# Performance work log

Hardware: AMD Instinct MI355X
Metric: run time of the kernel (lower is better)

## Reference

```python
import jax, jax.numpy as jnp
import numpy as np

N, F_IN, C, H, L = 4096, 768, 256, 4, 2
DH = C // H  # 64 per-head dim for GATv2


def _ln(x, g, b, eps=1e-5):
    mu = x.mean(-1, keepdims=True)
    var = ((x - mu) ** 2).mean(-1, keepdims=True)
    return (x - mu) / jnp.sqrt(var + eps) * g + b


def _gat_layer(x, wl, wr, att, b, src, dst):
    # GATv2Conv: e_ij = att . leaky_relu(Wl x_j + Wr x_i); softmax over incoming j; concat heads.
    xs = (x @ wl).reshape(N, H, DH)  # source transform
    xd = (x @ wr).reshape(N, H, DH)  # target transform
    e = jnp.einsum('ehd,hd->eh', jax.nn.leaky_relu(xs[src] + xd[dst], 0.2), att)  # [E,H]
    m = jax.ops.segment_max(e, dst, num_segments=N)          # segment softmax (stable)
    p = jnp.exp(e - m[dst])
    s = jax.ops.segment_sum(p, dst, num_segments=N)
    alpha = p / (s[dst] + 1e-16)                             # [E,H]
    out = jax.ops.segment_sum(alpha[:, :, None] * xs[src], dst, num_segments=N)
    return out.reshape(N, C) + b


def _mha(x, wq, wk, wv, bq, bk, bv, wo, bo):
    # nn.MultiheadAttention, batch=1 sequence of all news nodes, eval mode.
    q = (x @ wq + bq).reshape(N, H, DH)
    k = (x @ wk + bk).reshape(N, H, DH)
    v = (x @ wv + bv).reshape(N, H, DH)
    scale = np.float32(1.0 / np.sqrt(DH))
    a = jax.nn.softmax(jnp.einsum('nhd,mhd->hnm', q, k) * scale, axis=-1)  # [H,N,N]
    o = jnp.einsum('hnm,mhd->nhd', a, v).reshape(N, C)
    return o @ wo + bo


def setup_inputs() -> dict:
    key = jax.random.key(0)
    ks = jax.random.split(key, 32)
    rn = lambda k, shp: (jax.random.normal(k, shp, dtype=jnp.float32) * 0.02)
    inp = {
        'x': jax.random.normal(ks[0], (N, F_IN), dtype=jnp.float32),
        'edge_index': jax.random.randint(ks[1], (2, N * 64), 0, N, dtype=jnp.int64),
        'emb_w': rn(ks[2], (F_IN, C)), 'emb_b': jnp.zeros((C,), jnp.float32),
        'g1_wl': rn(ks[3], (C, C)), 'g1_wr': rn(ks[4], (C, C)),
        'g1_att': rn(ks[5], (H, DH)), 'g1_b': jnp.zeros((C,), jnp.float32),
        'g2_wl': rn(ks[6], (C, C)), 'g2_wr': rn(ks[7], (C, C)),
        'g2_att': rn(ks[8], (H, DH)), 'g2_b': jnp.zeros((C,), jnp.float32),
        'mha_wq': rn(ks[9], (C, C)), 'mha_wk': rn(ks[10], (C, C)), 'mha_wv': rn(ks[11], (C, C)),
        'mha_bq': jnp.zeros((C,), jnp.float32), 'mha_bk': jnp.zeros((C,), jnp.float32),
        'mha_bv': jnp.zeros((C,), jnp.float32),
        'mha_wo': rn(ks[12], (C, C)), 'mha_bo': jnp.zeros((C,), jnp.float32),
        'ln_g': jnp.ones((C,), jnp.float32), 'ln_b': jnp.zeros((C,), jnp.float32),
        'cls_w1': rn(ks[13], (C, C // 2)), 'cls_b1': jnp.zeros((C // 2,), jnp.float32),
        'cls_w2': rn(ks[14], (C // 2, 2)), 'cls_b2': jnp.zeros((2,), jnp.float32),
    }
    return inp


def reference(x, edge_index, emb_w, emb_b, g1_wl, g1_wr, g1_att, g1_b,
              g2_wl, g2_wr, g2_att, g2_b, mha_wq, mha_wk, mha_wv, mha_bq,
              mha_bk, mha_bv, mha_wo, mha_bo, ln_g, ln_b,
              cls_w1, cls_b1, cls_w2, cls_b2):
    # add self loops (GATv2Conv default add_self_loops=True)
    loops = jnp.arange(N, dtype=edge_index.dtype)
    src = jnp.concatenate([edge_index[0], loops])
    dst = jnp.concatenate([edge_index[1], loops])

    h = x @ emb_w + emb_b                              # node embedding Linear(-1, C)
    h = jax.nn.relu(_gat_layer(h, g1_wl, g1_wr, g1_att, g1_b, src, dst))
    h = jax.nn.relu(_gat_layer(h, g2_wl, g2_wr, g2_att, g2_b, src, dst))

    # entity-aware self-attention + residual LayerNorm
    enh = _mha(h, mha_wq, mha_wk, mha_wv, mha_bq, mha_bk, mha_bv, mha_wo, mha_bo)
    h = _ln(h + enh, ln_g, ln_b)

    # classifier MLP (dropout = identity in eval)
    h = jax.nn.relu(h @ cls_w1 + cls_b1)
    return h @ cls_w2 + cls_b2
```

## Files before the change

kernel.cpp:

```cpp
#include <hip/hip_runtime.h>

typedef __attribute__((ext_vector_type(8))) short short8_t;
typedef __attribute__((ext_vector_type(4))) short short4_t;
typedef __attribute__((ext_vector_type(4))) float f32x4_t;

#define N_NODES  4096
#define E0_EDGES 262144
#define E_TOTAL  266240
#define SPLITS   8
#define KV_PER_SPLIT (N_NODES / SPLITS)

__device__ __forceinline__ float bf2f(unsigned short u){
  union { unsigned int i; float f; } v; v.i = ((unsigned int)u) << 16; return v.f;
}
__device__ __forceinline__ unsigned short f2bf(float f){
  union { float f; unsigned int i; } v; v.f = f;
  unsigned int r = (v.i + 0x7FFFu + ((v.i >> 16) & 1u)) >> 16;
  return (unsigned short)r;
}
__device__ __forceinline__ unsigned int cvtpk_bf16(float lo, float hi){
  unsigned int r;
  asm volatile("v_cvt_pk_bf16_f32 %0, %1, %2" : "=v"(r) : "v"(lo), "v"(hi));
  return r;
}
template<int CTRL>
__device__ __forceinline__ float dpp_add(float x){
  int v = __builtin_amdgcn_update_dpp(0, __float_as_int(x), CTRL, 0xF, 0xF, true);
  return x + __int_as_float(v);
}
__device__ __forceinline__ float rowsum16(float x){
  x = dpp_add<0xB1>(x); x = dpp_add<0x4E>(x); x = dpp_add<0x124>(x); x = dpp_add<0x128>(x);
  return x;
}
__device__ __forceinline__ void wg_barrier(){
  asm volatile("s_waitcnt lgkmcnt(0)" ::: "memory");
  __builtin_amdgcn_s_barrier();
  asm volatile("" ::: "memory");
}
__device__ __forceinline__ f32x4_t mfma16(short4_t a, short4_t b, f32x4_t c){
  asm("v_mfma_f32_16x16x16_bf16 %0, %1, %2, %0" : "+v"(c) : "v"(a), "v"(b));
  return c;
}

struct TJob { const float* src; unsigned short* dst; int rows, cols, tile0; };
struct TJobs { TJob j[10]; };

__global__ __launch_bounds__(256) void prep_kernel(const float* __restrict__ x, unsigned short* __restrict__ xb,
                                                   TJobs jobs, int tb, int* __restrict__ zp){
  __shared__ unsigned short tile[64 * 64];
  int b = blockIdx.x, t = threadIdx.x;
  if (b < 3072){
    int i = (b * 256 + t) * 4;
    float4 v = *(const float4*)&x[i];
    union { unsigned short u[4]; uint2 q; } o;
    o.u[0] = f2bf(v.x); o.u[1] = f2bf(v.y); o.u[2] = f2bf(v.z); o.u[3] = f2bf(v.w);
    *(uint2*)&xb[i] = o.q;
    return;
  }
  if (b < 3072 + tb){
    int bb = b - 3072;
    int ji = 0;
    #pragma unroll
    for (int k = 1; k < 10; k++) if (bb >= jobs.j[k].tile0) ji = k;
    TJob J = jobs.j[ji];
    int lt = bb - J.tile0;
    int tpr = J.cols >> 6;
    int tr = lt / tpr, tc = lt - tr * tpr;
    #pragma unroll
    for (int i2 = 0; i2 < 2; i2++){
      int e = i2 * 2048 + t * 8;
      int nl = e >> 6, c8 = e & 63;
      const float* sp = &J.src[(size_t)(tr * 64 + nl) * J.cols + tc * 64 + c8];
      float4 v0 = *(const float4*)sp;
      float4 v1 = *(const float4*)(sp + 4);
      union { unsigned short u[8]; uint4 q; } o;
      o.u[0]=f2bf(v0.x); o.u[1]=f2bf(v0.y); o.u[2]=f2bf(v0.z); o.u[3]=f2bf(v0.w);
      o.u[4]=f2bf(v1.x); o.u[5]=f2bf(v1.y); o.u[6]=f2bf(v1.z); o.u[7]=f2bf(v1.w);
      *(uint4*)&tile[nl * 64 + (((c8 >> 3) ^ ((nl >> 3) & 7)) * 8)] = o.q;
    }
    __syncthreads();
    #pragma unroll
    for (int i2 = 0; i2 < 2; i2++){
      int e = i2 * 2048 + t * 8;
      int cl = e >> 6, n8 = e & 63;
      union { unsigned short u[8]; uint4 q; } o;
      #pragma unroll
      for (int j = 0; j < 8; j++){
        int row = n8 + j;
        o.u[j] = tile[row * 64 + (((cl >> 3) ^ ((row >> 3) & 7)) * 8) + (cl & 7)];
      }
      *(uint4*)&J.dst[(size_t)(tc * 64 + cl) * J.rows + tr * 64 + n8] = o.q;
    }
    return;
  }
  int i = (b - 3072 - tb) * 256 + t;
  if (i < 8192) zp[i] = 0;
}

__global__ __launch_bounds__(256) void scatter_kernel(const int* __restrict__ ei, const int* __restrict__ offs,
                                                      int* __restrict__ cur, int* __restrict__ csrc){
  int e = blockIdx.x * 256 + threadIdx.x;
  if (e >= E_TOTAL) return;
  int s, d;
  if (e < E0_EDGES){ s = ei[e]; d = ei[E0_EDGES + e]; }
  else { s = d = e - E0_EDGES; }
  int pos = offs[d] + atomicAdd(&cur[d], 1);
  csrc[pos] = s;
}

struct GJob { const unsigned short* Wt; const float* bias; float* outF; unsigned short* outB; unsigned short* outT; float scale; };
struct GJobs { GJob j[3]; };
struct AuxJob { int mode; const int* ei; int* a; int* b; };

__global__ __launch_bounds__(256) void gemm_kernel(const unsigned short* __restrict__ A, GJobs jobs,
                                                   int K, int Nc, int relu, AuxJob AX){
  __shared__ unsigned short lds[8192];
  const int t = threadIdx.x;

  if (AX.mode && blockIdx.z == gridDim.z - 1){
    int flat = blockIdx.x + (blockIdx.y << 6);
    if (AX.mode == 1){
      for (int e = flat * 256 + t; e < E_TOTAL; e += 65536){
        int d = (e < E0_EDGES) ? AX.ei[E0_EDGES + e] : (e - E0_EDGES);
        atomicAdd(&AX.a[d], 1);
      }
    } else if (flat == 0){
      int* wtot = (int*)lds;
      int lane = t & 63, w = t >> 6;
      int v[16];
      int base = t * 16;
      int s = 0;
      #pragma unroll
      for (int j = 0; j < 16; j++){ v[j] = AX.a[base + j]; s += v[j]; }
      int x = s;
      #pragma unroll
      for (int off = 1; off < 64; off <<= 1){
        int y = __shfl_up(x, off, 64);
        if (lane >= off) x += y;
      }
      if (lane == 63) wtot[w] = x;
      __syncthreads();
      int wbase = 0;
      #pragma unroll
      for (int k = 0; k < 4; k++) if (k < w) wbase += wtot[k];
      int run = wbase + x - s;
      #pragma unroll
      for (int j = 0; j < 16; j++){ AX.b[base + j] = run; run += v[j]; }
      if (t == 255) AX.b[N_NODES] = run;
    }
    return;
  }

  const GJob job = jobs.j[blockIdx.z];
  const int lane = t & 63, w = t >> 6;
  const int wm = w >> 1, wn = w & 1;
  const int c16 = lane & 15, g = lane >> 4;
  const int bm = blockIdx.x, bn = blockIdx.y;

  const int srow = t >> 2, schunk = t & 3;
  const unsigned short* Ag = A      + (size_t)(bm * 64 + srow) * K + schunk * 8;
  const unsigned short* Bg = job.Wt + (size_t)(bn * 64 + srow) * K + schunk * 8;
  const int swz = srow * 32 + ((schunk ^ ((srow >> 1) & 3)) * 8);

  const int arow0 = wm * 32 + c16, arow1 = arow0 + 16;
  const int aoff0 = arow0 * 32 + ((g ^ ((arow0 >> 1) & 3)) * 8);
  const int aoff1 = arow1 * 32 + ((g ^ ((arow1 >> 1) & 3)) * 8);
  const int bcol0 = wn * 32 + c16, bcol1 = bcol0 + 16;
  const int boff0 = 2048 + bcol0 * 32 + ((g ^ ((bcol0 >> 1) & 3)) * 8);
  const int boff1 = 2048 + bcol1 * 32 + ((g ^ ((bcol1 >> 1) & 3)) * 8);

  f32x4_t acc[2][2] = {};
  const int nk = K >> 5;

  {
    uint4 av = *(const uint4*)(Ag);
    uint4 bv = *(const uint4*)(Bg);
    *(uint4*)&lds[swz]        = av;
    *(uint4*)&lds[2048 + swz] = bv;
  }
  int cur = 0;
  for (int i = 0; i < nk; i++){
    const bool pf = (i + 1) < nk;
    uint4 av, bv;
    if (pf){
      av = *(const uint4*)(Ag + (i + 1) * 32);
      bv = *(const uint4*)(Bg + (i + 1) * 32);
    }
    wg_barrier();
    const int base = cur * 4096;
    union { uint4 u; short8_t s; } a0, a1, b0, b1;
    a0.u = *(const uint4*)&lds[base + aoff0];
    a1.u = *(const uint4*)&lds[base + aoff1];
    b0.u = *(const uint4*)&lds[base + boff0];
    b1.u = *(const uint4*)&lds[base + boff1];
    acc[0][0] = __builtin_amdgcn_mfma_f32_16x16x32_bf16(a0.s, b0.s, acc[0][0], 0, 0, 0);
    acc[0][1] = __builtin_amdgcn_mfma_f32_16x16x32_bf16(a0.s, b1.s, acc[0][1], 0, 0, 0);
    acc[1][0] = __builtin_amdgcn_mfma_f32_16x16x32_bf16(a1.s, b0.s, acc[1][0], 0, 0, 0);
    acc[1][1] = __builtin_amdgcn_mfma_f32_16x16x32_bf16(a1.s, b1.s, acc[1][1], 0, 0, 0);
    if (pf){
      const int nb = (cur ^ 1) * 4096;
      *(uint4*)&lds[nb + swz]        = av;
      *(uint4*)&lds[nb + 2048 + swz] = bv;
      cur ^= 1;
    }
  }

  #pragma unroll
  for (int fm = 0; fm < 2; fm++){
    #pragma unroll
    for (int fn = 0; fn < 2; fn++){
      int col = bn * 64 + wn * 32 + fn * 16 + c16;
      float bia = job.bias ? job.bias[col] : 0.f;
      float vv[4];
      #pragma unroll
      for (int r = 0; r < 4; r++){
        float v = (acc[fm][fn][r] + bia) * job.scale;
        if (relu) v = fmaxf(v, 0.f);
        vv[r] = v;
      }
      int row0 = bm * 64 + wm * 32 + fm * 16 + g * 4;
      if (job.outF){
        #pragma unroll
        for (int r = 0; r < 4; r++) job.outF[(size_t)(row0 + r) * Nc + col] = vv[r];
      }
      if (job.outB){
        #pragma unroll
        for (int r = 0; r < 4; r++) job.outB[(size_t)(row0 + r) * Nc + col] = f2bf(vv[r]);
      }
      if (job.outT){
        union { unsigned short u[4]; uint2 q; } pk;
        #pragma unroll
        for (int r = 0; r < 4; r++) pk.u[r] = f2bf(vv[r]);
        *(uint2*)&job.outT[(size_t)col * 4096 + row0] = pk.q;
      }
    }
  }
}

__global__ __launch_bounds__(256) void gat_gather(const unsigned short* __restrict__ xs, const unsigned short* __restrict__ xd,
                                                  const float* __restrict__ att, const float* __restrict__ bias,
                                                  const int* __restrict__ offs, const int* __restrict__ csrc,
                                                  unsigned short* __restrict__ outB, float* __restrict__ outF){
  __shared__ float combL[4][256];
  __shared__ float combS[4][4];
  const int i = blockIdx.x, t = threadIdx.x;
  const int lane = t & 63, w = t >> 6;
  float xdc[4], attc[4];
  {
    uint2 xv = *(const uint2*)&xd[i * 256 + lane * 4];
    xdc[0] = bf2f((unsigned short)(xv.x & 0xffff)); xdc[1] = bf2f((unsigned short)(xv.x >> 16));
    xdc[2] = bf2f((unsigned short)(xv.y & 0xffff)); xdc[3] = bf2f((unsigned short)(xv.y >> 16));
    float4 av = *(const float4*)&att[lane * 4];
    attc[0] = av.x; attc[1] = av.y; attc[2] = av.z; attc[3] = av.w;
  }
  const int b0 = offs[i], b1 = offs[i + 1];
  float acc0 = 0.f, acc1 = 0.f, acc2 = 0.f, acc3 = 0.f, ssum = 0.f;
  int p = b0 + w;
  for (; p + 4 < b1; p += 8){
    int sA = csrc[p], sB = csrc[p + 4];
    uint2 xa = *(const uint2*)&xs[sA * 256 + lane * 4];
    uint2 xb = *(const uint2*)&xs[sB * 256 + lane * 4];
    float a0 = bf2f((unsigned short)(xa.x & 0xffff)), a1 = bf2f((unsigned short)(xa.x >> 16));
    float a2 = bf2f((unsigned short)(xa.y & 0xffff)), a3 = bf2f((unsigned short)(xa.y >> 16));
    float b0_ = bf2f((unsigned short)(xb.x & 0xffff)), b1_ = bf2f((unsigned short)(xb.x >> 16));
    float b2_ = bf2f((unsigned short)(xb.y & 0xffff)), b3_ = bf2f((unsigned short)(xb.y >> 16));
    float va0 = a0 + xdc[0]; va0 = (va0 > 0.f) ? va0 : 0.2f * va0;
    float va1 = a1 + xdc[1]; va1 = (va1 > 0.f) ? va1 : 0.2f * va1;
    float va2 = a2 + xdc[2]; va2 = (va2 > 0.f) ? va2 : 0.2f * va2;
    float va3 = a3 + xdc[3]; va3 = (va3 > 0.f) ? va3 : 0.2f * va3;
    float vb0 = b0_ + xdc[0]; vb0 = (vb0 > 0.f) ? vb0 : 0.2f * vb0;
    float vb1 = b1_ + xdc[1]; vb1 = (vb1 > 0.f) ? vb1 : 0.2f * vb1;
    float vb2 = b2_ + xdc[2]; vb2 = (vb2 > 0.f) ? vb2 : 0.2f * vb2;
    float vb3 = b3_ + xdc[3]; vb3 = (vb3 > 0.f) ? vb3 : 0.2f * vb3;
    float eA = rowsum16(va0 * attc[0] + va1 * attc[1] + va2 * attc[2] + va3 * attc[3]);
    float eB = rowsum16(vb0 * attc[0] + vb1 * attc[1] + vb2 * attc[2] + vb3 * attc[3]);
    float pA = __expf(eA), pB = __expf(eB);
    ssum += pA + pB;
    acc0 += pA * a0 + pB * b0_; acc1 += pA * a1 + pB * b1_;
    acc2 += pA * a2 + pB * b2_; acc3 += pA * a3 + pB * b3_;
  }
  if (p < b1){
    int s = csrc[p];
    uint2 xv = *(const uint2*)&xs[s * 256 + lane * 4];
    float x0 = bf2f((unsigned short)(xv.x & 0xffff)), x1 = bf2f((unsigned short)(xv.x >> 16));
    float x2 = bf2f((unsigned short)(xv.y & 0xffff)), x3 = bf2f((unsigned short)(xv.y >> 16));
    float v0 = x0 + xdc[0]; v0 = (v0 > 0.f) ? v0 : 0.2f * v0;
    float v1 = x1 + xdc[1]; v1 = (v1 > 0.f) ? v1 : 0.2f * v1;
    float v2 = x2 + xdc[2]; v2 = (v2 > 0.f) ? v2 : 0.2f * v2;
    float v3 = x3 + xdc[3]; v3 = (v3 > 0.f) ? v3 : 0.2f * v3;
    float e = rowsum16(v0 * attc[0] + v1 * attc[1] + v2 * attc[2] + v3 * attc[3]);
    float pe = __expf(e);
    ssum += pe;
    acc0 += pe * x0; acc1 += pe * x1; acc2 += pe * x2; acc3 += pe * x3;
  }
  combL[w][lane * 4 + 0] = acc0; combL[w][lane * 4 + 1] = acc1;
  combL[w][lane * 4 + 2] = acc2; combL[w][lane * 4 + 3] = acc3;
  if ((lane & 15) == 0) combS[w][lane >> 4] = ssum;
  __syncthreads();
  float atot = combL[0][t] + combL[1][t] + combL[2][t] + combL[3][t];
  int hh = t >> 6;
  float stot = combS[0][hh] + combS[1][hh] + combS[2][hh] + combS[3][hh];
  float o = atot / (stot + 1e-16f) + bias[t];
  o = fmaxf(o, 0.f);
  outB[i * 256 + t] = f2bf(o);
  if (outF) outF[i * 256 + t] = o;
}

__global__ __launch_bounds__(256, 4) void attn_kernel(const unsigned short* __restrict__ qb, const unsigned short* __restrict__ kb,
                                                      const unsigned short* __restrict__ vt,
                                                      float* __restrict__ Opart, float* __restrict__ Ol){
  __shared__ unsigned short K_lds[2][4096];
  __shared__ unsigned short V_lds[2][4096];
  const int t = threadIdx.x, lane = t & 63, w = t >> 6;
  const int c16 = lane & 15, g = lane >> 4;
  const int h = blockIdx.y, bq = blockIdx.x, sp = blockIdx.z;

  const int e0 = t * 8, e1 = 2048 + t * 8;
  const int sr0 = e0 >> 6, sc0 = e0 & 63;
  const int sr1 = e1 >> 6, sc1 = e1 & 63;
  const int kw0 = sr0 * 64 + (((sc0 >> 3) ^ ((sr0 >> 1) & 7)) * 8);
  const int kw1 = sr1 * 64 + (((sc1 >> 3) ^ ((sr1 >> 1) & 7)) * 8);
  const int vw0 = sr0 * 64 + (((sc0 >> 3) ^ (sr0 & 7)) * 8);
  const int vw1 = sr1 * 64 + (((sc1 >> 3) ^ (sr1 & 7)) * 8);

  short8_t qa[2][2];
  #pragma unroll
  for (int qm = 0; qm < 2; qm++){
    int qrow = bq * 128 + w * 32 + qm * 16 + c16;
    union { uint4 u; short8_t s; } cv0, cv1;
    cv0.u = *(const uint4*)&qb[(size_t)qrow * 256 + h * 64 + g * 8];
    cv1.u = *(const uint4*)&qb[(size_t)qrow * 256 + h * 64 + 32 + g * 8];
    qa[qm][0] = cv0.s; qa[qm][1] = cv1.s;
  }

  f32x4_t oacc[2][4] = {};
  float lsum[2] = {0.f, 0.f};

  const int kv_lo = sp * KV_PER_SPLIT;
  {
    uint4 k0 = *(const uint4*)&kb[(size_t)(kv_lo + sr0) * 256 + h * 64 + sc0];
    uint4 k1 = *(const uint4*)&kb[(size_t)(kv_lo + sr1) * 256 + h * 64 + sc1];
    uint4 v0 = *(const uint4*)&vt[(size_t)(h * 64 + sr0) * 4096 + kv_lo + sc0];
    uint4 v1 = *(const uint4*)&vt[(size_t)(h * 64 + sr1) * 4096 + kv_lo + sc1];
    *(uint4*)&K_lds[0][kw0] = k0; *(uint4*)&K_lds[0][kw1] = k1;
    *(uint4*)&V_lds[0][vw0] = v0; *(uint4*)&V_lds[0][vw1] = v1;
  }
  int cur = 0;

  for (int ti = 0; ti < KV_PER_SPLIT / 64; ti++){
    const bool pf = (ti + 1) < KV_PER_SPLIT / 64;
    uint4 nk0, nk1, nv0, nv1;
    if (pf){
      int kvn = kv_lo + (ti + 1) * 64;
      nk0 = *(const uint4*)&kb[(size_t)(kvn + sr0) * 256 + h * 64 + sc0];
      nk1 = *(const uint4*)&kb[(size_t)(kvn + sr1) * 256 + h * 64 + sc1];
      nv0 = *(const uint4*)&vt[(size_t)(h * 64 + sr0) * 4096 + kvn + sc0];
      nv1 = *(const uint4*)&vt[(size_t)(h * 64 + sr1) * 4096 + kvn + sc1];
    }
    wg_barrier();
    const unsigned short* Kb = K_lds[cur];
    const unsigned short* Vb = V_lds[cur];

    f32x4_t sacc[2][4] = {};
    #pragma unroll
    for (int kd = 0; kd < 2; kd++){
      #pragma unroll
      for (int fn = 0; fn < 4; fn++){
        union { uint4 u; short8_t s; } kf;
        kf.u = *(const uint4*)&Kb[(fn * 16 + c16) * 64 + (((kd * 4 + g) ^ ((c16 >> 1) & 7)) * 8)];
        sacc[0][fn] = __builtin_amdgcn_mfma_f32_16x16x32_bf16(kf.s, qa[0][kd], sacc[0][fn], 0, 0, 0);
        sacc[1][fn] = __builtin_amdgcn_mfma_f32_16x16x32_bf16(kf.s, qa[1][kd], sacc[1][fn], 0, 0, 0);
      }
    }

    short4_t pfr[2][4];
    #pragma unroll
    for (int qm = 0; qm < 2; qm++){
      float ps = 0.f;
      #pragma unroll
      for (int fn = 0; fn < 4; fn++){
        float p0 = __expf(sacc[qm][fn][0]);
        float p1 = __expf(sacc[qm][fn][1]);
        float p2 = __expf(sacc[qm][fn][2]);
        float p3 = __expf(sacc[qm][fn][3]);
        ps += (p0 + p1) + (p2 + p3);
        union { uint2 u; short4_t s; } pk;
        pk.u.x = cvtpk_bf16(p0, p1);
        pk.u.y = cvtpk_bf16(p2, p3);
        pfr[qm][fn] = pk.s;
      }
      ps += __shfl_xor(ps, 16, 64);
      ps += __shfl_xor(ps, 32, 64);
      lsum[qm] += ps;
    }

    #pragma unroll
    for (int fnkv = 0; fnkv < 4; fnkv++){
      const int chb = fnkv * 2 + (g >> 1);
      #pragma unroll
      for (int fd = 0; fd < 4; fd++){
        int row = fd * 16 + c16;
        union { uint2 u; short4_t s; } vf;
        vf.u = *(const uint2*)&Vb[row * 64 + ((chb ^ (row & 7)) * 8) + (g & 1) * 4];
        oacc[0][fd] = mfma16(vf.s, pfr[0][fnkv], oacc[0][fd]);
        oacc[1][fd] = mfma16(vf.s, pfr[1][fnkv], oacc[1][fd]);
      }
    }

    if (pf){
      *(uint4*)&K_lds[cur ^ 1][kw0] = nk0; *(uint4*)&K_lds[cur ^ 1][kw1] = nk1;
      *(uint4*)&V_lds[cur ^ 1][vw0] = nv0; *(uint4*)&V_lds[cur ^ 1][vw1] = nv1;
      cur ^= 1;
    }
  }

  const int sh = sp * 4 + h;
  #pragma unroll
  for (int qm = 0; qm < 2; qm++){
    int node = bq * 128 + w * 32 + qm * 16 + c16;
    #pragma unroll
    for (int fd = 0; fd < 4; fd++){
      *(float4*)&Opart[((size_t)sh * N_NODES + node) * 64 + fd * 16 + g * 4] =
        *(float4*)&oacc[qm][fd];
    }
    if (g == 0) Ol[(size_t)sh * N_NODES + node] = lsum[qm];
  }
}

__global__ __launch_bounds__(256) void wo_ln_cls_kernel(const float* __restrict__ Opart, const float* __restrict__ Ol,
                                                        const unsigned short* __restrict__ Wt, const float* __restrict__ bo,
                                                        const float* __restrict__ h2f, const float* __restrict__ gg,
                                                        const float* __restrict__ bb,
                                                        const unsigned short* __restrict__ Wt1, const float* __restrict__ b1,
                                                        const float* __restrict__ w2, const float* __restrict__ b2,
                                                        float* __restrict__ out){
  __shared__ unsigned short Ab[2][512];
  __shared__ unsigned short Bb[2][8192];
  __shared__ unsigned short Cb[2][4096];
  __shared__ unsigned short hl[16 * 264];
  __shared__ float red1[4][16], red2[4][16];
  __shared__ float cred0[4][16], cred1[4][16];
  __shared__ float Ls[64];
  const int t = threadIdx.x, lane = t & 63, w = t >> 6;
  const int c16 = lane & 15, g = lane >> 4;
  const int bm = blockIdx.x;

  const int arow = t >> 2, achk = t & 3;
  const int aswz = arow * 32 + ((achk ^ ((arow >> 1) & 3)) * 8);
  const int bq_ = t >> 2, bchk = t & 3;

  if (t < 64){
    int node = bm * 16 + (t >> 2), h = t & 3;
    float L = 0.f;
    #pragma unroll
    for (int s = 0; s < SPLITS; s++) L += Ol[(size_t)(s * 4 + h) * N_NODES + node];
    Ls[t] = 1.f / L;
  }
  __syncthreads();

  const int afr = c16 * 32 + ((g ^ ((c16 >> 1) & 3)) * 8);
  int bfr[4];
  #pragma unroll
  for (int fn = 0; fn < 4; fn++){
    int col = w * 64 + fn * 16 + c16;
    bfr[fn] = col * 32 + ((g ^ ((col >> 1) & 3)) * 8);
  }

  const int anode = bm * 16 + arow;
  auto loadA = [&](int k0, float4* pa){
    int c0 = k0 + achk * 8;
    int hh = c0 >> 6, d0 = c0 & 63;
    #pragma unroll
    for (int s = 0; s < SPLITS; s++){
      const float* bp = &Opart[((size_t)(s * 4 + hh) * N_NODES + anode) * 64 + d0];
      pa[s * 2]     = *(const float4*)bp;
      pa[s * 2 + 1] = *(const float4*)(bp + 4);
    }
  };
  auto packA = [&](int k0, const float4* pa) -> uint4 {
    float a[8] = {0.f,0.f,0.f,0.f,0.f,0.f,0.f,0.f};
    #pragma unroll
    for (int s = 0; s < SPLITS; s++){
      a[0] += pa[s*2].x;   a[1] += pa[s*2].y;   a[2] += pa[s*2].z;   a[3] += pa[s*2].w;
      a[4] += pa[s*2+1].x; a[5] += pa[s*2+1].y; a[6] += pa[s*2+1].z; a[7] += pa[s*2+1].w;
    }
    int c0 = k0 + achk * 8;
    float Li = Ls[(arow << 2) | (c0 >> 6)];
    union { unsigned short u[8]; uint4 q; } o;
    #pragma unroll
    for (int j = 0; j < 8; j++) o.u[j] = f2bf(a[j] * Li);
    return o.q;
  };

  f32x4_t acc[4] = {};
  {
    if (t < 64){
      float4 pa0[SPLITS * 2];
      loadA(0, pa0);
      *(uint4*)&Ab[0][aswz] = packA(0, pa0);
    }
    #pragma unroll
    for (int j = 0; j < 4; j++){
      int col = j * 64 + bq_;
      *(uint4*)&Bb[0][col * 32 + ((bchk ^ ((col >> 1) & 3)) * 8)] = *(const uint4*)&Wt[(size_t)col * 256 + bchk * 8];
    }
  }
  int cur = 0;
  for (int i = 0; i < 8; i++){
    const bool pf = i < 7;
    float4 pa[SPLITS * 2]; uint4 pb[4];
    int k1 = (i + 1) * 32;
    if (pf){
      if (t < 64) loadA(k1, pa);
      #pragma unroll
      for (int j = 0; j < 4; j++){
        int col = j * 64 + bq_;
        pb[j] = *(const uint4*)&Wt[(size_t)col * 256 + k1 + bchk * 8];
      }
    }
    wg_barrier();
    union { uint4 u; short8_t s; } a, b;
    a.u = *(const uint4*)&Ab[cur][afr];
    #pragma unroll
    for (int fn = 0; fn < 4; fn++){
      b.u = *(const uint4*)&Bb[cur][bfr[fn]];
      acc[fn] = __builtin_amdgcn_mfma_f32_16x16x32_bf16(a.s, b.s, acc[fn], 0, 0, 0);
    }
    if (pf){
      if (t < 64) *(uint4*)&Ab[cur ^ 1][aswz] = packA(k1, pa);
      #pragma unroll
      for (int j = 0; j < 4; j++){
        int col = j * 64 + bq_;
        *(uint4*)&Bb[cur ^ 1][col * 32 + ((bchk ^ ((col >> 1) & 3)) * 8)] = pb[j];
      }
      cur ^= 1;
    }
  }

  float vv[4][4];
  #pragma unroll
  for (int fn = 0; fn < 4; fn++){
    int col = w * 64 + fn * 16 + c16;
    float bia = bo[col];
    #pragma unroll
    for (int r = 0; r < 4; r++)
      vv[fn][r] = acc[fn][r] + bia + h2f[(size_t)(bm * 16 + g * 4 + r) * 256 + col];
  }
  #pragma unroll
  for (int r = 0; r < 4; r++){
    float a = 0.f, b = 0.f;
    #pragma unroll
    for (int fn = 0; fn < 4; fn++){ a += vv[fn][r]; b += vv[fn][r] * vv[fn][r]; }
    a = rowsum16(a); b = rowsum16(b);
    if (c16 == 0){ red1[w][g * 4 + r] = a; red2[w][g * 4 + r] = b; }
  }
  __syncthreads();
  #pragma unroll
  for (int r = 0; r < 4; r++){
    int row = g * 4 + r;
    float S1 = red1[0][row] + red1[1][row] + red1[2][row] + red1[3][row];
    float S2 = red2[0][row] + red2[1][row] + red2[2][row] + red2[3][row];
    float mean = S1 * (1.f / 256.f);
    float var = S2 * (1.f / 256.f) - mean * mean;
    float rs = rsqrtf(var + 1e-5f);
    #pragma unroll
    for (int fn = 0; fn < 4; fn++){
      int col = w * 64 + fn * 16 + c16;
      hl[row * 264 + col] = f2bf((vv[fn][r] - mean) * rs * gg[col] + bb[col]);
    }
  }

  wg_barrier();
  int cfr[2];
  #pragma unroll
  for (int fn = 0; fn < 2; fn++){
    int col = w * 32 + fn * 16 + c16;
    cfr[fn] = col * 32 + ((g ^ ((col >> 1) & 3)) * 8);
  }
  f32x4_t cacc[2] = {};
  {
    #pragma unroll
    for (int j = 0; j < 2; j++){
      int col = j * 64 + bq_;
      *(uint4*)&Cb[0][col * 32 + ((bchk ^ ((col >> 1) & 3)) * 8)] = *(const uint4*)&Wt1[(size_t)col * 256 + bchk * 8];
    }
  }
  cur = 0;
  for (int i = 0; i < 8; i++){
    const bool pf = i < 7;
    uint4 pb[2];
    if (pf){
      int k1 = (i + 1) * 32;
      #pragma unroll
      for (int j = 0; j < 2; j++){
        int col = j * 64 + bq_;
        pb[j] = *(const uint4*)&Wt1[(size_t)col * 256 + k1 + bchk * 8];
      }
    }
    wg_barrier();
    union { uint4 u; short8_t s; } a, b;
    a.u = *(const uint4*)&hl[c16 * 264 + i * 32 + g * 8];
    #pragma unroll
    for (int fn = 0; fn < 2; fn++){
      b.u = *(const uint4*)&Cb[cur][cfr[fn]];
      cacc[fn] = __builtin_amdgcn_mfma_f32_16x16x32_bf16(a.s, b.s, cacc[fn], 0, 0, 0);
    }
    if (pf){
      #pragma unroll
      for (int j = 0; j < 2; j++){
        int col = j * 64 + bq_;
        *(uint4*)&Cb[cur ^ 1][col * 32 + ((bchk ^ ((col >> 1) & 3)) * 8)] = pb[j];
      }
      cur ^= 1;
    }
  }
  float cv[2][4];
  #pragma unroll
  for (int fn = 0; fn < 2; fn++){
    int col = w * 32 + fn * 16 + c16;
    float bia = b1[col];
    #pragma unroll
    for (int r = 0; r < 4; r++) cv[fn][r] = fmaxf(cacc[fn][r] + bia, 0.f);
  }
  float w20 = w2[(w * 32 + c16) * 2],      w21 = w2[(w * 32 + c16) * 2 + 1];
  float w30 = w2[(w * 32 + 16 + c16) * 2], w31 = w2[(w * 32 + 16 + c16) * 2 + 1];
  #pragma unroll
  for (int r = 0; r < 4; r++){
    float a0 = cv[0][r] * w20 + cv[1][r] * w30;
    float a1 = cv[0][r] * w21 + cv[1][r] * w31;
    a0 = rowsum16(a0); a1 = rowsum16(a1);
    if (c16 == 0){ cred0[w][g * 4 + r] = a0; cred1[w][g * 4 + r] = a1; }
  }
  __syncthreads();
  if (t < 16){
    float q0 = cred0[0][t] + cred0[1][t] + cred0[2][t] + cred0[3][t] + b2[0];
    float q1 = cred1[0][t] + cred1[1][t] + cred1[2][t] + cred1[3][t] + b2[1];
    out[(size_t)(bm * 16 + t) * 2]     = q0;
    out[(size_t)(bm * 16 + t) * 2 + 1] = q1;
  }
}

extern "C" void kernel_launch(void* const* d_in, const int* in_sizes, int n_in,
                              void* d_out, int out_size, void* d_ws, size_t ws_size,
                              hipStream_t stream){
  const float* x      = (const float*)d_in[0];
  const int*   ei     = (const int*)d_in[1];
  const float* emb_w  = (const float*)d_in[2];
  const float* emb_b  = (const float*)d_in[3];
  const float* g1_wl  = (const float*)d_in[4];
  const float* g1_wr  = (const float*)d_in[5];
  const float* g1_att = (const float*)d_in[6];
  const float* g1_b   = (const float*)d_in[7];
  const float* g2_wl  = (const float*)d_in[8];
  const float* g2_wr  = (const float*)d_in[9];
  const float* g2_att = (const float*)d_in[10];
  const float* g2_b   = (const float*)d_in[11];
  const float* wq     = (const float*)d_in[12];
  const float* wk     = (const float*)d_in[13];
  const float* wv     = (const float*)d_in[14];
  const float* bq     = (const float*)d_in[15];
  const float* bk     = (const float*)d_in[16];
  const float* bv     = (const float*)d_in[17];
  const float* wo     = (const float*)d_in[18];
  const float* bo     = (const float*)d_in[19];
  const float* ln_g   = (const float*)d_in[20];
  const float* ln_b   = (const float*)d_in[21];
  const float* cls_w1 = (const float*)d_in[22];
  const float* cls_b1 = (const float*)d_in[23];
  const float* cls_w2 = (const float*)d_in[24];
  const float* cls_b2 = (const float*)d_in[25];
  float* out = (float*)d_out;

  char* wsb = (char*)d_ws;
  size_t o = 0;
  auto take = [&](size_t bytes) -> char* {
    char* r = wsb + o; o += (bytes + 255) & ~(size_t)255; return r;
  };
  unsigned short* wt_emb  = (unsigned short*)take(768 * 256 * 2);
  unsigned short* wt_wl1  = (unsigned short*)take(256 * 256 * 2);
  unsigned short* wt_wr1  = (unsigned short*)take(256 * 256 * 2);
  unsigned short* wt_wl2  = (unsigned short*)take(256 * 256 * 2);
  unsigned short* wt_wr2  = (unsigned short*)take(256 * 256 * 2);
  unsigned short* wt_wq   = (unsigned short*)take(256 * 256 * 2);
  unsigned short* wt_wk   = (unsigned short*)take(256 * 256 * 2);
  unsigned short* wt_wv   = (unsigned short*)take(256 * 256 * 2);
  unsigned short* wt_wo   = (unsigned short*)take(256 * 256 * 2);
  unsigned short* wt_cls1 = (unsigned short*)take(256 * 128 * 2);
  unsigned short* x_bf    = (unsigned short*)take((size_t)4096 * 768 * 2);
  unsigned short* h0_bf   = (unsigned short*)take((size_t)4096 * 256 * 2);
  unsigned short* xs1_bf  = (unsigned short*)take((size_t)4096 * 256 * 2);
  unsigned short* xd1_bf  = (unsigned short*)take((size_t)4096 * 256 * 2);
  unsigned short* h1_bf   = (unsigned short*)take((size_t)4096 * 256 * 2);
  unsigned short* xs2_bf  = (unsigned short*)take((size_t)4096 * 256 * 2);
  unsigned short* xd2_bf  = (unsigned short*)take((size_t)4096 * 256 * 2);
  unsigned short* h2_bf   = (unsigned short*)take((size_t)4096 * 256 * 2);
  float*          h2_f    = (float*)take((size_t)4096 * 256 * 4);
  unsigned short* q_bf    = (unsigned short*)take((size_t)4096 * 256 * 2);
  unsigned short* k_bf    = (unsigned short*)take((size_t)4096 * 256 * 2);
  unsigned short* vt_bf   = (unsigned short*)take((size_t)4096 * 256 * 2);
  int* deg  = (int*)take(4096 * 4);
  int* cur  = (int*)take(4096 * 4);
  int* offs = (int*)take(4097 * 4);
  int* csrc = (int*)take((size_t)E_TOTAL * 4);
  float* Opart = (float*)take((size_t)SPLITS * 4 * N_NODES * 64 * 4);
  float* Ol    = (float*)take((size_t)SPLITS * 4 * N_NODES * 4);

  TJobs TJ;
  TJob tj[10] = {
    { emb_w,  wt_emb,  768, 256, 0 },
    { g1_wl,  wt_wl1,  256, 256, 0 },
    { g1_wr,  wt_wr1,  256, 256, 0 },
    { g2_wl,  wt_wl2,  256, 256, 0 },
    { g2_wr,  wt_wr2,  256, 256, 0 },
    { wq,     wt_wq,   256, 256, 0 },
    { wk,     wt_wk,   256, 256, 0 },
    { wv,     wt_wv,   256, 256, 0 },
    { wo,     wt_wo,   256, 256, 0 },
    { cls_w1, wt_cls1, 256, 128, 0 },
  };
  int tb = 0;
  for (int i = 0; i < 10; i++){
    tj[i].tile0 = tb;
    tb += (tj[i].rows >> 6) * (tj[i].cols >> 6);
    TJ.j[i] = tj[i];
  }
  prep_kernel<<<3072 + tb + 32, 256, 0, stream>>>(x, x_bf, TJ, tb, deg);

  GJobs J;
  AuxJob AX0 = { 0, nullptr, nullptr, nullptr };
  J = {}; J.j[0] = { wt_emb, emb_b, nullptr, h0_bf, nullptr, 1.f };
  AuxJob AXh = { 1, ei, deg, nullptr };
  gemm_kernel<<<dim3(64, 4, 2), 256, 0, stream>>>(x_bf, J, 768, 256, 0, AXh);
  J = {}; J.j[0] = { wt_wl1, nullptr, nullptr, xs1_bf, nullptr, 1.f }; J.j[1] = { wt_wr1, nullptr, nullptr, xd1_bf, nullptr, 1.f };
  AuxJob AXs = { 2, nullptr, deg, offs };
  gemm_kernel<<<dim3(64, 4, 3), 256, 0, stream>>>(h0_bf, J, 256, 256, 0, AXs);
  scatter_kernel<<<(E_TOTAL + 255) / 256, 256, 0, stream>>>(ei, offs, cur, csrc);
  gat_gather<<<4096, 256, 0, stream>>>(xs1_bf, xd1_bf, g1_att, g1_b, offs, csrc, h1_bf, nullptr);
  J = {}; J.j[0] = { wt_wl2, nullptr, nullptr, xs2_bf, nullptr, 1.f }; J.j[1] = { wt_wr2, nullptr, nullptr, xd2_bf, nullptr, 1.f };
  gemm_kernel<<<dim3(64, 4, 2), 256, 0, stream>>>(h1_bf, J, 256, 256, 0, AX0);
  gat_gather<<<4096, 256, 0, stream>>>(xs2_bf, xd2_bf, g2_att, g2_b, offs, csrc, h2_bf, h2_f);
  J = {};
  J.j[0] = { wt_wq, bq, nullptr, q_bf, nullptr, 0.125f };
  J.j[1] = { wt_wk, bk, nullptr, k_bf, nullptr, 1.f };
  J.j[2] = { wt_wv, bv, nullptr, nullptr, vt_bf, 1.f };
  gemm_kernel<<<dim3(64, 4, 3), 256, 0, stream>>>(h2_bf, J, 256, 256, 0, AX0);
  attn_kernel<<<dim3(32, 4, SPLITS), 256, 0, stream>>>(q_bf, k_bf, vt_bf, Opart, Ol);
  wo_ln_cls_kernel<<<256, 256, 0, stream>>>(Opart, Ol, wt_wo, bo, h2_f, ln_g, ln_b,
                                            wt_cls1, cls_b1, cls_w2, cls_b2, out);

  (void)in_sizes; (void)n_in; (void)out_size; (void)ws_size;
}
```

Baseline: 173.3 us.

## Widen attention workgroups to 512 threads and stage P through LDS for 16x16x32 MFMA

The attention kernel now runs 8 waves per workgroup (256 queries per block, half as many blocks), so each K/V tile loaded into LDS is shared by twice as many query rows. Each thread loads one 16-byte chunk of K and V instead of two. The softmax probabilities are written to a per-wave swizzled LDS buffer and read back as 8-wide fragments, which lets the PV product use the 16x16x32 bf16 MFMA instead of the 16x16x16 one. In exchange the kernel adds LDS writes and reads for P, uses 32KB more LDS, and has fewer, larger blocks, which lowers occupancy flexibility.

New measurement: 162.2 us. 1.07x faster.

```diff
diff --git a/kernel.cpp b/kernel.cpp
--- a/kernel.cpp
+++ b/kernel.cpp
@@ -1,7 +1,6 @@
 #include <hip/hip_runtime.h>
 
 typedef __attribute__((ext_vector_type(8))) short short8_t;
-typedef __attribute__((ext_vector_type(4))) short short4_t;
 typedef __attribute__((ext_vector_type(4))) float f32x4_t;
 
 #define N_NODES  4096
@@ -36,10 +35,6 @@
   asm volatile("s_waitcnt lgkmcnt(0)" ::: "memory");
   __builtin_amdgcn_s_barrier();
   asm volatile("" ::: "memory");
-}
-__device__ __forceinline__ f32x4_t mfma16(short4_t a, short4_t b, f32x4_t c){
-  asm("v_mfma_f32_16x16x16_bf16 %0, %1, %2, %0" : "+v"(c) : "v"(a), "v"(b));
-  return c;
 }
 
 struct TJob { const float* src; unsigned short* dst; int rows, cols, tile0; };
@@ -306,27 +301,24 @@
   if (outF) outF[i * 256 + t] = o;
 }
 
-__global__ __launch_bounds__(256, 4) void attn_kernel(const unsigned short* __restrict__ qb, const unsigned short* __restrict__ kb,
+__global__ __launch_bounds__(512, 2) void attn_kernel(const unsigned short* __restrict__ qb, const unsigned short* __restrict__ kb,
                                                       const unsigned short* __restrict__ vt,
                                                       float* __restrict__ Opart, float* __restrict__ Ol){
   __shared__ unsigned short K_lds[2][4096];
   __shared__ unsigned short V_lds[2][4096];
+  __shared__ unsigned short P_lds[8][2048];
   const int t = threadIdx.x, lane = t & 63, w = t >> 6;
   const int c16 = lane & 15, g = lane >> 4;
   const int h = blockIdx.y, bq = blockIdx.x, sp = blockIdx.z;
 
-  const int e0 = t * 8, e1 = 2048 + t * 8;
-  const int sr0 = e0 >> 6, sc0 = e0 & 63;
-  const int sr1 = e1 >> 6, sc1 = e1 & 63;
-  const int kw0 = sr0 * 64 + (((sc0 >> 3) ^ ((sr0 >> 1) & 7)) * 8);
-  const int kw1 = sr1 * 64 + (((sc1 >> 3) ^ ((sr1 >> 1) & 7)) * 8);
-  const int vw0 = sr0 * 64 + (((sc0 >> 3) ^ (sr0 & 7)) * 8);
-  const int vw1 = sr1 * 64 + (((sc1 >> 3) ^ (sr1 & 7)) * 8);
+  const int sr = t >> 3, sc = (t & 7) * 8;
+  const int kw = sr * 64 + (((t & 7) ^ ((sr >> 1) & 7)) * 8);
+  const int vw = sr * 64 + (((t & 7) ^ (sr & 7)) * 8);
 
   short8_t qa[2][2];
   #pragma unroll
   for (int qm = 0; qm < 2; qm++){
-    int qrow = bq * 128 + w * 32 + qm * 16 + c16;
+    int qrow = bq * 256 + w * 32 + qm * 16 + c16;
     union { uint4 u; short8_t s; } cv0, cv1;
     cv0.u = *(const uint4*)&qb[(size_t)qrow * 256 + h * 64 + g * 8];
     cv1.u = *(const uint4*)&qb[(size_t)qrow * 256 + h * 64 + 32 + g * 8];
@@ -338,28 +330,25 @@
 
   const int kv_lo = sp * KV_PER_SPLIT;
   {
-    uint4 k0 = *(const uint4*)&kb[(size_t)(kv_lo + sr0) * 256 + h * 64 + sc0];
-    uint4 k1 = *(const uint4*)&kb[(size_t)(kv_lo + sr1) * 256 + h * 64 + sc1];
-    uint4 v0 = *(const uint4*)&vt[(size_t)(h * 64 + sr0) * 4096 + kv_lo + sc0];
-    uint4 v1 = *(const uint4*)&vt[(size_t)(h * 64 + sr1) * 4096 + kv_lo + sc1];
-    *(uint4*)&K_lds[0][kw0] = k0; *(uint4*)&K_lds[0][kw1] = k1;
-    *(uint4*)&V_lds[0][vw0] = v0; *(uint4*)&V_lds[0][vw1] = v1;
+    uint4 k0 = *(const uint4*)&kb[(size_t)(kv_lo + sr) * 256 + h * 64 + sc];
+    uint4 v0 = *(const uint4*)&vt[(size_t)(h * 64 + sr) * 4096 + kv_lo + sc];
+    *(uint4*)&K_lds[0][kw] = k0;
+    *(uint4*)&V_lds[0][vw] = v0;
   }
   int cur = 0;
 
   for (int ti = 0; ti < KV_PER_SPLIT / 64; ti++){
     const bool pf = (ti + 1) < KV_PER_SPLIT / 64;
-    uint4 nk0, nk1, nv0, nv1;
+    uint4 nk, nv;
     if (pf){
       int kvn = kv_lo + (ti + 1) * 64;
-      nk0 = *(const uint4*)&kb[(size_t)(kvn + sr0) * 256 + h * 64 + sc0];
-      nk1 = *(const uint4*)&kb[(size_t)(kvn + sr1) * 256 + h * 64 + sc1];
-      nv0 = *(const uint4*)&vt[(size_t)(h * 64 + sr0) * 4096 + kvn + sc0];
-      nv1 = *(const uint4*)&vt[(size_t)(h * 64 + sr1) * 4096 + kvn + sc1];
+      nk = *(const uint4*)&kb[(size_t)(kvn + sr) * 256 + h * 64 + sc];
+      nv = *(const uint4*)&vt[(size_t)(h * 64 + sr) * 4096 + kvn + sc];
     }
     wg_barrier();
     const unsigned short* Kb = K_lds[cur];
     const unsigned short* Vb = V_lds[cur];
+    unsigned short* Pw = P_lds[w];
 
     f32x4_t sacc[2][4] = {};
     #pragma unroll
@@ -373,10 +362,10 @@
       }
     }
 
-    short4_t pfr[2][4];
     #pragma unroll
     for (int qm = 0; qm < 2; qm++){
       float ps = 0.f;
+      int row = qm * 16 + c16;
       #pragma unroll
       for (int fn = 0; fn < 4; fn++){
         float p0 = __expf(sacc[qm][fn][0]);
@@ -384,10 +373,11 @@
         float p2 = __expf(sacc[qm][fn][2]);
         float p3 = __expf(sacc[qm][fn][3]);
         ps += (p0 + p1) + (p2 + p3);
-        union { uint2 u; short4_t s; } pk;
-        pk.u.x = cvtpk_bf16(p0, p1);
-        pk.u.y = cvtpk_bf16(p2, p3);
-        pfr[qm][fn] = pk.s;
+        uint2 pk;
+        pk.x = cvtpk_bf16(p0, p1);
+        pk.y = cvtpk_bf16(p2, p3);
+        int chunk = (fn * 2 + (g >> 1)) ^ (c16 & 7);
+        *(uint2*)&Pw[row * 64 + chunk * 8 + (g & 1) * 4] = pk;
       }
       ps += __shfl_xor(ps, 16, 64);
       ps += __shfl_xor(ps, 32, 64);
@@ -395,21 +385,23 @@
     }
 
     #pragma unroll
-    for (int fnkv = 0; fnkv < 4; fnkv++){
-      const int chb = fnkv * 2 + (g >> 1);
-      #pragma unroll
-      for (int fd = 0; fd < 4; fd++){
-        int row = fd * 16 + c16;
-        union { uint2 u; short4_t s; } vf;
-        vf.u = *(const uint2*)&Vb[row * 64 + ((chb ^ (row & 7)) * 8) + (g & 1) * 4];
-        oacc[0][fd] = mfma16(vf.s, pfr[0][fnkv], oacc[0][fd]);
-        oacc[1][fd] = mfma16(vf.s, pfr[1][fnkv], oacc[1][fd]);
+    for (int kd2 = 0; kd2 < 2; kd2++){
+      const int ch = (((kd2 * 4 + g) ^ (c16 & 7)) * 8);
+      union { uint4 u; short8_t s; } pt0, pt1;
+      pt0.u = *(const uint4*)&Pw[c16 * 64 + ch];
+      pt1.u = *(const uint4*)&Pw[(16 + c16) * 64 + ch];
+      #pragma unroll
+      for (int fn = 0; fn < 4; fn++){
+        union { uint4 u; short8_t s; } vf;
+        vf.u = *(const uint4*)&Vb[(fn * 16 + c16) * 64 + ch];
+        oacc[0][fn] = __builtin_amdgcn_mfma_f32_16x16x32_bf16(vf.s, pt0.s, oacc[0][fn], 0, 0, 0);
+        oacc[1][fn] = __builtin_amdgcn_mfma_f32_16x16x32_bf16(vf.s, pt1.s, oacc[1][fn], 0, 0, 0);
       }
     }
 
     if (pf){
-      *(uint4*)&K_lds[cur ^ 1][kw0] = nk0; *(uint4*)&K_lds[cur ^ 1][kw1] = nk1;
-      *(uint4*)&V_lds[cur ^ 1][vw0] = nv0; *(uint4*)&V_lds[cur ^ 1][vw1] = nv1;
+      *(uint4*)&K_lds[cur ^ 1][kw] = nk;
+      *(uint4*)&V_lds[cur ^ 1][vw] = nv;
       cur ^= 1;
     }
   }
@@ -417,11 +409,11 @@
   const int sh = sp * 4 + h;
   #pragma unroll
   for (int qm = 0; qm < 2; qm++){
-    int node = bq * 128 + w * 32 + qm * 16 + c16;
-    #pragma unroll
-    for (int fd = 0; fd < 4; fd++){
-      *(float4*)&Opart[((size_t)sh * N_NODES + node) * 64 + fd * 16 + g * 4] =
-        *(float4*)&oacc[qm][fd];
+    int node = bq * 256 + w * 32 + qm * 16 + c16;
+    #pragma unroll
+    for (int fn = 0; fn < 4; fn++){
+      *(float4*)&Opart[((size_t)sh * N_NODES + node) * 64 + fn * 16 + g * 4] =
+        *(float4*)&oacc[qm][fn];
     }
     if (g == 0) Ol[(size_t)sh * N_NODES + node] = lsum[qm];
   }
@@ -744,7 +736,7 @@
   J.j[1] = { wt_wk, bk, nullptr, k_bf, nullptr, 1.f };
   J.j[2] = { wt_wv, bv, nullptr, nullptr, vt_bf, 1.f };
   gemm_kernel<<<dim3(64, 4, 3), 256, 0, stream>>>(h2_bf, J, 256, 256, 0, AX0);
-  attn_kernel<<<dim3(32, 4, SPLITS), 256, 0, stream>>>(q_bf, k_bf, vt_bf, Opart, Ol);
+  attn_kernel<<<dim3(16, 4, SPLITS), 512, 0, stream>>>(q_bf, k_bf, vt_bf, Opart, Ol);
   wo_ln_cls_kernel<<<256, 256, 0, stream>>>(Opart, Ol, wt_wo, bo, h2_f, ln_g, ln_b,
                                             wt_cls1, cls_b1, cls_w2, cls_b2, out);
 
```
